# Kernel tuning notes

Measured on AMD Instinct MI355X. Metric: run time of the kernel, lower is better.

The kernel has to match this reference:

```python
import jax, jax.numpy as jnp
import numpy as np

N = 100000
NNZ = 1600000
DIM = 128
IN_FEAT = 128


def spmm(vals, rows, cols, x, n):
    # sparse [n,n] COO @ dense [n,d] -> [n,d]
    return jax.ops.segment_sum(vals[:, None] * x[cols], rows, num_segments=n)


def setup_inputs() -> dict:
    key = jax.random.key(0)
    ks = jax.random.split(key, 7)
    inputs = jax.random.normal(ks[0], (N, IN_FEAT), dtype=jnp.float32)
    # TruncatedNormal(stddev=1/sqrt(fan_in)) approximated by scaled normal
    w1 = jax.random.normal(ks[1], (N, DIM), dtype=jnp.float32) / np.sqrt(N)
    w2 = jax.random.normal(ks[2], (IN_FEAT, DIM), dtype=jnp.float32) / np.sqrt(IN_FEAT)
    wg = jax.random.normal(ks[3], (DIM, 1), dtype=jnp.float32)  # glorot-ish, dim=1 gate
    A_vals = jax.random.uniform(ks[4], (NNZ,), dtype=jnp.float32)
    A_rows = jax.random.randint(ks[5], (NNZ,), 0, N, dtype=jnp.int32)
    A_cols = jax.random.randint(ks[6], (NNZ,), 0, N, dtype=jnp.int32)
    return {"inputs": inputs, "w1": w1, "w2": w2, "wg": wg,
            "A_vals": A_vals, "A_rows": A_rows, "A_cols": A_cols}


def reference(inputs, w1, w2, wg, A_vals, A_rows, A_cols):
    n = w1.shape[0]
    # aw layer: relu(A @ w1)
    a = jax.nn.relu(spmm(A_vals, A_rows, A_cols, w1, n))          # [N, dim]
    # axw layer: relu(A @ (X @ w2))
    b = jax.nn.relu(spmm(A_vals, A_rows, A_cols, inputs @ w2, n))  # [N, dim]
    # highway gate: T = sigmoid(b @ wg); y = T*a + (1-T)*b
    T = jax.nn.sigmoid(b @ wg)                                     # [N, 1]
    y = T * a + (1.0 - T) * b                                      # [N, dim]
    # final propagation: A @ y
    return spmm(A_vals, A_rows, A_cols, y, n)
```

## Files before the change

kernel.cpp:

```cpp
#include <hip/hip_runtime.h>
#include <hip/hip_bf16.h>
#include <hip/hip_fp16.h>


using f16x8 = __attribute__((ext_vector_type(8))) _Float16;
using f32x4 = __attribute__((ext_vector_type(4))) float;
using f32x2 = __attribute__((ext_vector_type(2))) float;

#define W1SCALE 128.0f
#define VSCL    3.0517578125e-05f
#define AF      (VSCL / 128.0f)
#define CHUNK   4096
#define BROWS   512
#define BSHIFT  9
#define MAXNB   256

__device__ __forceinline__ int block_incl_scan(int v, int* wsum) {
  int tid = threadIdx.x, lane = tid & 63, wid = tid >> 6;
  int incl = v;
#pragma unroll
  for (int off = 1; off < 64; off <<= 1) {
    int t = __shfl_up(incl, off);
    if (lane >= off) incl += t;
  }
  if (lane == 63) wsum[wid] = incl;
  __syncthreads();
  if (wid == 0) {
    int nw = (int)(blockDim.x >> 6);
    int wv = (lane < nw) ? wsum[lane] : 0;
    int wi = wv;
#pragma unroll
    for (int off = 1; off < 16; off <<= 1) {
      int t = __shfl_up(wi, off);
      if (lane >= off) wi += t;
    }
    if (lane < nw) wsum[lane] = wi - wv;
  }
  __syncthreads();
  return incl + wsum[wid];
}

__global__ __launch_bounds__(256) void k_colscan(const int* __restrict__ partials,
                                                 int* __restrict__ colscanT,
                                                 int* __restrict__ bktfill,
                                                 int nb, int sb) {
  int lane = threadIdx.x & 63, w = threadIdx.x >> 6;
  int b = blockIdx.x * 4 + w;
  if (b >= nb) return;
  int carry = 0;
  for (int ci0 = 0; ci0 < sb; ci0 += 64) {
    int ci = ci0 + lane;
    int v = (ci < sb) ? partials[(size_t)ci * nb + b] : 0;
    int incl = v;
#pragma unroll
    for (int off = 1; off < 64; off <<= 1) {
      int t = __shfl_up(incl, off);
      if (lane >= off) incl += t;
    }
    if (ci < sb) colscanT[(size_t)b * sb + ci] = carry + incl - v;
    carry += __shfl(incl, 63);
  }
  if (lane == 0) bktfill[b] = carry;
}

__global__ __launch_bounds__(1024) void k_sortscan(const int* __restrict__ bktfill,
                                                   int* __restrict__ bktbase,
                                                   int nb, int* __restrict__ rp,
                                                   int n, int nnz) {
  __shared__ int wsum[16];
  int tid = threadIdx.x;
  int v = (tid < nb) ? bktfill[tid] : 0;
  int incl = block_incl_scan(v, wsum);
  if (tid < nb) bktbase[tid] = incl - v;
  if (tid == 0) rp[n] = nnz;
}

__global__ __launch_bounds__(256) void k_scatter3(const int* __restrict__ Ar,
                                                  const int* __restrict__ Ac,
                                                  const float* __restrict__ Av,
                                                  const int* __restrict__ colscanT,
                                                  uint2* __restrict__ tmp,
                                                  int nnz, int nb, int cap, int sb) {
  __shared__ int cursor[MAXNB];
  int tid = threadIdx.x, bi = blockIdx.x;
  for (int t = tid; t < nb; t += 256)
    cursor[t] = t * cap + colscanT[(size_t)t * sb + bi];
  __syncthreads();
  int base = bi * CHUNK;
  int cnt = min(CHUNK, nnz - base);
  for (int it = 0; it < CHUNK / 256; ++it) {
    int k = it * 256 + tid;
    if (k < cnt) {
      int i = base + k;
      int r = Ar[i];
      int bkt = r >> BSHIFT;
      unsigned uq = (unsigned)fminf(Av[i] * 32768.f + 0.5f, 32767.f);
      int pos = atomicAdd(&cursor[bkt], 1);
      if (pos < (bkt + 1) * cap)
        tmp[pos] = make_uint2(((unsigned)Ac[i] << 15) | uq, (unsigned)r);
    }
  }
}

__global__ __launch_bounds__(1024) void k_sort3(const uint2* __restrict__ tmp,
                                                const int* __restrict__ bktfill,
                                                const int* __restrict__ bktbase,
                                                unsigned* __restrict__ ccv,
                                                int* __restrict__ rp,
                                                int n, int cap) {
  __shared__ int rcnt[BROWS];
  __shared__ int rbase[BROWS];
  int b = blockIdx.x, tid = threadIdx.x;
  int cnt = min(bktfill[b], cap);
  const uint2* src = tmp + (size_t)b * cap;
  int bbase = bktbase[b];
  if (tid < BROWS) rcnt[tid] = 0;
  __syncthreads();

  for (int i = tid; i < cnt; i += 1024)
    atomicAdd(&rcnt[src[i].y & (BROWS - 1)], 1);
  __syncthreads();

  int own = (tid < BROWS) ? rcnt[tid] : 0;
  for (int off = 1; off < BROWS; off <<= 1) {
    int v = 0;
    if (tid < BROWS) {
      v = rcnt[tid];
      if (tid >= off) v += rcnt[tid - off];
    }
    __syncthreads();
    if (tid < BROWS) rcnt[tid] = v;
    __syncthreads();
  }
  if (tid < BROWS) {
    int ex = rcnt[tid] - own;
    rbase[tid] = ex;
    int row = b * BROWS + tid;
    if (row < n) rp[row] = bbase + ex;
  }
  __syncthreads();
  if (tid < BROWS) rcnt[tid] = rbase[tid];
  __syncthreads();

  for (int i = tid; i < cnt; i += 1024) {
    uint2 rr = src[i];
    int p = atomicAdd(&rcnt[rr.y & (BROWS - 1)], 1);
    ccv[bbase + p] = rr.x;
  }
}

#define BM 256
__global__ __launch_bounds__(256) void k_gemm(const float* __restrict__ X,
                                              const float* __restrict__ w1,
                                              const float* __restrict__ W,
                                              __half* __restrict__ xw16,
                                              unsigned char* __restrict__ w1f8, int n,
                                              const int* __restrict__ Ar,
                                              int* __restrict__ partials,
                                              int nnz, int nb, int sortB) {
  __shared__ char smem[32768];
  int tid = threadIdx.x;

  if (blockIdx.x < sortB) {
    int* hist = (int*)smem;
    int bi = blockIdx.x;
    int base = bi * CHUNK;
    int cnt = min(CHUNK, nnz - base);
    for (int t = tid; t < nb; t += 256) hist[t] = 0;
    __syncthreads();
    for (int it = 0; it < CHUNK / 256; ++it) {
      int k = it * 256 + tid;
      if (k < cnt) atomicAdd(&hist[Ar[base + k] >> BSHIFT], 1);
    }
    __syncthreads();
    for (int t = tid; t < nb; t += 256)
      partials[(size_t)bi * nb + t] = hist[t];
    return;
  }

  __half* lds = (__half*)smem;
  for (int t = tid; t < 2048; t += 256) {
    int nn = t >> 4, kg = t & 15;
    union { _Float16 h[8]; uint4 u; } u;
#pragma unroll
    for (int j = 0; j < 8; ++j) u.h[j] = (_Float16)W[(kg * 8 + j) * 128 + nn];
    int byte = nn * 256 + ((kg * 16) ^ ((nn & 7) << 4));
    *(uint4*)((char*)lds + byte) = u.u;
  }

  long r0 = (long)(blockIdx.x - sortB) * BM;
  for (int i = tid; i < BM * 16; i += 256) {
    int rr = i >> 4, gg = i & 15;
    long r = r0 + rr;
    if (r < n) {
      const float* src = w1 + r * 128 + gg * 8;
      float4 f0 = *(const float4*)src;
      float4 f1 = *(const float4*)(src + 4);
      int lo = __builtin_amdgcn_cvt_pk_fp8_f32(f0.x * W1SCALE, f0.y * W1SCALE, 0, false);
      lo = __builtin_amdgcn_cvt_pk_fp8_f32(f0.z * W1SCALE, f0.w * W1SCALE, lo, true);
      int hi = __builtin_amdgcn_cvt_pk_fp8_f32(f1.x * W1SCALE, f1.y * W1SCALE, 0, false);
      hi = __builtin_amdgcn_cvt_pk_fp8_f32(f1.z * W1SCALE, f1.w * W1SCALE, hi, true);
      uint2 st = {(unsigned)lo, (unsigned)hi};
      *(uint2*)(w1f8 + r * 128 + gg * 8) = st;
    }
  }
  __syncthreads();

  int wid = tid >> 6, lane = tid & 63;
  int g = lane >> 4, lm = lane & 15;
  long rowbase = r0 + wid * 64;

  f16x8 afr[4][4];
#pragma unroll
  for (int m = 0; m < 4; ++m) {
    long r = rowbase + m * 16 + lm;
    if (r >= n) r = n - 1;
    const float* xp = X + r * 128 + g * 8;
#pragma unroll
    for (int kk = 0; kk < 4; ++kk) {
      float4 lo = *(const float4*)(xp + kk * 32);
      float4 hi = *(const float4*)(xp + kk * 32 + 4);
      f16x8 a;
      a[0] = (_Float16)lo.x; a[1] = (_Float16)lo.y;
      a[2] = (_Float16)lo.z; a[3] = (_Float16)lo.w;
      a[4] = (_Float16)hi.x; a[5] = (_Float16)hi.y;
      a[6] = (_Float16)hi.z; a[7] = (_Float16)hi.w;
      afr[m][kk] = a;
    }
  }

#pragma unroll
  for (int nt = 0; nt < 8; ++nt) {
    int nn = nt * 16 + lm;
    int sw = (nn & 7) << 4;
    f16x8 bfr[4];
#pragma unroll
    for (int kk = 0; kk < 4; ++kk) {
      int byte = nn * 256 + ((kk * 64 + g * 16) ^ sw);
      bfr[kk] = *(f16x8*)((char*)lds + byte);
    }
#pragma unroll
    for (int m = 0; m < 4; ++m) {
      f32x4 acc = {0.f, 0.f, 0.f, 0.f};
#pragma unroll
      for (int kk = 0; kk < 4; ++kk)
        acc = __builtin_amdgcn_mfma_f32_16x16x32_f16(afr[m][kk], bfr[kk], acc, 0, 0, 0);
#pragma unroll
      for (int r = 0; r < 4; ++r) {
        long row = rowbase + m * 16 + g * 4 + r;
        if (row < n) xw16[row * 128 + nn] = __float2half(acc[r]);
      }
    }
  }
}

__global__ __launch_bounds__(256) void k_spmm_ab(const int* __restrict__ rp,
                                                 const unsigned* __restrict__ ccv,
                                                 const unsigned char* __restrict__ w1f8,
                                                 const __half* __restrict__ xw16,
                                                 const float* __restrict__ wg,
                                                 unsigned char* __restrict__ y8,
                                                 float* __restrict__ yscl, int n) {
  int row = (int)((blockIdx.x * 256 + threadIdx.x) >> 6);
  int lane = threadIdx.x & 63;
  if (row >= n) return;
  int s = rp[row], e = rp[row + 1];
  const unsigned char* aptr = w1f8 + lane * 2;
  const __half* bptr = xw16 + lane * 2;
  float aa0 = 0.f, aa1 = 0.f, bb0 = 0.f, bb1 = 0.f;

#define AB_EDGE(J)                                                         \
  {                                                                        \
    unsigned mm = (unsigned)__builtin_amdgcn_readlane((int)mr, (J));       \
    unsigned col = mm >> 15;                                               \
    float vq = (float)(mm & 0x7fffu);                                      \
    unsigned ua = *(const unsigned short*)(aptr + (size_t)col * 128);      \
    unsigned ub = *(const unsigned*)((const char*)bptr + (size_t)col * 256); \
    f32x2 fa = __builtin_amdgcn_cvt_pk_f32_fp8(ua, false);                 \
    float2 fb = __half22float2(*(__half2*)&ub);                            \
    aa0 = fmaf(vq, fa[0], aa0); aa1 = fmaf(vq, fa[1], aa1);                \
    bb0 = fmaf(vq, fb.x, bb0); bb1 = fmaf(vq, fb.y, bb1);                  \
  }

  for (int chunk = s; chunk < e; chunk += 64) {
    int idx = chunk + lane;
    unsigned mr = (idx < e) ? ccv[idx] : 0u;
    int cl = min(64, e - chunk);
    int j = 0;
    for (; j + 3 < cl; j += 4) {
      AB_EDGE(j) AB_EDGE(j + 1) AB_EDGE(j + 2) AB_EDGE(j + 3)
    }
    for (; j < cl; ++j) AB_EDGE(j)
  }
#undef AB_EDGE

  float a0 = fmaxf(aa0 * AF, 0.f), a1 = fmaxf(aa1 * AF, 0.f);
  float b0 = fmaxf(bb0 * VSCL, 0.f), b1 = fmaxf(bb1 * VSCL, 0.f);

  float2 wgv = *(const float2*)(wg + lane * 2);
  float part = b0 * wgv.x + b1 * wgv.y;
#pragma unroll
  for (int off = 32; off > 0; off >>= 1) part += __shfl_xor(part, off);
  float T = 1.f / (1.f + __expf(-part));
  float u = 1.f - T;

  float y0 = T * a0 + u * b0;
  float y1 = T * a1 + u * b1;

  float m = fmaxf(y0, y1);
#pragma unroll
  for (int off = 32; off > 0; off >>= 1) m = fmaxf(m, __shfl_xor(m, off));
  float scl = (m > 0.f) ? 255.f / m : 0.f;
  unsigned q0 = min((unsigned)(y0 * scl + 0.5f), 255u);
  unsigned q1 = min((unsigned)(y1 * scl + 0.5f), 255u);
  *(unsigned short*)(y8 + (size_t)row * 128 + lane * 2) =
      (unsigned short)(q0 | (q1 << 8));
  if (lane == 0) yscl[row] = m * (1.f / 255.f);
}

__global__ __launch_bounds__(256) void k_spmm_out(const int* __restrict__ rp,
                                                  const unsigned* __restrict__ ccv,
                                                  const unsigned char* __restrict__ y8,
                                                  const float* __restrict__ yscl,
                                                  float* __restrict__ out, int n) {
  int row = (int)((blockIdx.x * 256 + threadIdx.x) >> 6);
  int lane = threadIdx.x & 63;
  if (row >= n) return;
  int s = rp[row], e = rp[row + 1];
  const unsigned char* ysub = y8 + lane * 2;
  float ac0 = 0.f, ac1 = 0.f;

#define OUT_EDGE(J)                                                        \
  {                                                                        \
    unsigned mm = (unsigned)__builtin_amdgcn_readlane((int)mr, (J));       \
    unsigned col = mm >> 15;                                               \
    float vs = (float)(mm & 0x7fffu) * yscl[col];                          \
    unsigned u = *(const unsigned short*)(ysub + (size_t)col * 128);       \
    ac0 = fmaf(vs, (float)(u & 255u), ac0);                                \
    ac1 = fmaf(vs, (float)(u >> 8), ac1);                                  \
  }

  for (int chunk = s; chunk < e; chunk += 64) {
    int idx = chunk + lane;
    unsigned mr = (idx < e) ? ccv[idx] : 0u;
    int cl = min(64, e - chunk);
    int j = 0;
    for (; j + 3 < cl; j += 4) {
      OUT_EDGE(j) OUT_EDGE(j + 1) OUT_EDGE(j + 2) OUT_EDGE(j + 3)
    }
    for (; j < cl; ++j) OUT_EDGE(j)
  }
#undef OUT_EDGE

  union { float2 f2; long long ll; } ov;
  ov.f2.x = ac0 * VSCL;
  ov.f2.y = ac1 * VSCL;
  __builtin_nontemporal_store(ov.ll, (long long*)(out + (size_t)row * 128 + lane * 2));
}

extern "C" void kernel_launch(void* const* d_in, const int* in_sizes, int n_in,
                              void* d_out, int out_size, void* d_ws, size_t ws_size,
                              hipStream_t stream) {
  const float* X  = (const float*)d_in[0];
  const float* w1 = (const float*)d_in[1];
  const float* w2 = (const float*)d_in[2];
  const float* wg = (const float*)d_in[3];
  const float* Av = (const float*)d_in[4];
  const int*   Ar = (const int*)d_in[5];
  const int*   Ac = (const int*)d_in[6];
  float* out = (float*)d_out;
  int N   = in_sizes[0] / 128;
  int NNZ = in_sizes[4];

  int NB    = (N + BROWS - 1) >> BSHIFT;
  int sortB = (NNZ + CHUNK - 1) / CHUNK;
  int cap   = (NNZ / NB) * 3 / 2 + 256;

  char* p = (char*)d_ws;
  auto alloc = [&](size_t b) {
    char* r = p;
    p += (b + 255) & ~(size_t)255;
    return r;
  };
  int*            rp       = (int*)alloc((size_t)(N + 1) * 4);
  int*            partials = (int*)alloc((size_t)sortB * NB * 4);
  int*            colscanT = (int*)alloc((size_t)NB * sortB * 4);
  int*            bktfill  = (int*)alloc((size_t)NB * 4);
  int*            bktbase  = (int*)alloc((size_t)NB * 4);
  uint2*          tmp      = (uint2*)alloc((size_t)NB * cap * 8);
  unsigned*       ccv      = (unsigned*)alloc((size_t)NNZ * 4);
  __half*         xw16     = (__half*)alloc((size_t)N * 128 * 2);
  unsigned char*  w1f8     = (unsigned char*)alloc((size_t)N * 128);
  unsigned char*  y8       = (unsigned char*)alloc((size_t)N * 128);
  float*          yscl     = (float*)alloc((size_t)N * 4);

  int gemmB = (N + BM - 1) / BM;
  k_gemm<<<sortB + gemmB, 256, 0, stream>>>(X, w1, w2, xw16, w1f8, N,
                                            Ar, partials, NNZ, NB, sortB);
  k_colscan<<<(NB + 3) / 4, 256, 0, stream>>>(partials, colscanT, bktfill, NB, sortB);
  k_sortscan<<<1, 1024, 0, stream>>>(bktfill, bktbase, NB, rp, N, NNZ);
  k_scatter3<<<sortB, 256, 0, stream>>>(Ar, Ac, Av, colscanT, tmp, NNZ, NB, cap, sortB);
  k_sort3<<<NB, 1024, 0, stream>>>(tmp, bktfill, bktbase, ccv, rp, N, cap);
  int wb = (N + 3) / 4;
  k_spmm_ab<<<wb, 256, 0, stream>>>(rp, ccv, w1f8, xw16, wg, y8, yscl, N);
  k_spmm_out<<<wb, 256, 0, stream>>>(rp, ccv, y8, yscl, out, N);
}
```

Before: 224.5 us.

## Stage bucket scatter in shared memory for coalesced global writes

The scatter kernel now builds a per-block bucket histogram, scans it, and first places each chunk's entries in LDS grouped by bucket. It then writes them out contiguously to global memory, so writes within a bucket are coalesced instead of scattered 8-byte stores. The cost is an extra pass reading Ar, a serial-ish shared-memory scan with many syncthreads, and 32KB of LDS per block, which may reduce occupancy.

```diff
diff --git a/kernel.cpp b/kernel.cpp
--- a/kernel.cpp
+++ b/kernel.cpp
@@ -81,13 +81,37 @@
                                                   const int* __restrict__ colscanT,
                                                   uint2* __restrict__ tmp,
                                                   int nnz, int nb, int cap, int sb) {
-  __shared__ int cursor[MAXNB];
+  __shared__ uint2 buf[CHUNK];
+  __shared__ int lhist[MAXNB];
+  __shared__ int lcur[MAXNB];
+  __shared__ int gbase[MAXNB];
   int tid = threadIdx.x, bi = blockIdx.x;
-  for (int t = tid; t < nb; t += 256)
-    cursor[t] = t * cap + colscanT[(size_t)t * sb + bi];
-  __syncthreads();
   int base = bi * CHUNK;
   int cnt = min(CHUNK, nnz - base);
+  for (int t = tid; t < nb; t += 256) lhist[t] = 0;
+  __syncthreads();
+  for (int it = 0; it < CHUNK / 256; ++it) {
+    int k = it * 256 + tid;
+    if (k < cnt) atomicAdd(&lhist[Ar[base + k] >> BSHIFT], 1);
+  }
+  __syncthreads();
+  int own = (tid < nb) ? lhist[tid] : 0;
+  for (int off = 1; off < nb; off <<= 1) {
+    int v = 0;
+    if (tid < nb) {
+      v = lhist[tid];
+      if (tid >= off) v += lhist[tid - off];
+    }
+    __syncthreads();
+    if (tid < nb) lhist[tid] = v;
+    __syncthreads();
+  }
+  if (tid < nb) {
+    int ex = lhist[tid] - own;
+    lcur[tid] = ex;
+    gbase[tid] = tid * cap + colscanT[(size_t)tid * sb + bi] - ex;
+  }
+  __syncthreads();
   for (int it = 0; it < CHUNK / 256; ++it) {
     int k = it * 256 + tid;
     if (k < cnt) {
@@ -95,9 +119,18 @@
       int r = Ar[i];
       int bkt = r >> BSHIFT;
       unsigned uq = (unsigned)fminf(Av[i] * 32768.f + 0.5f, 32767.f);
-      int pos = atomicAdd(&cursor[bkt], 1);
-      if (pos < (bkt + 1) * cap)
-        tmp[pos] = make_uint2(((unsigned)Ac[i] << 15) | uq, (unsigned)r);
+      int pos = atomicAdd(&lcur[bkt], 1);
+      buf[pos] = make_uint2(((unsigned)Ac[i] << 15) | uq, (unsigned)r);
+    }
+  }
+  __syncthreads();
+  for (int it = 0; it < CHUNK / 256; ++it) {
+    int i = it * 256 + tid;
+    if (i < cnt) {
+      uint2 rr = buf[i];
+      int bkt = (int)(rr.y >> BSHIFT);
+      int gp = gbase[bkt] + i;
+      if (gp < (bkt + 1) * cap) tmp[gp] = rr;
     }
   }
 }
```

New measurement: 225.0 us. Within noise of the previous version (+0.2%).
